# Kernel tuning notes

Hardware: AMD Instinct MI355X
Metric: run time of the kernel (lower is better)

Reference implementation:

```python
import jax, jax.numpy as jnp
import numpy as np

B, S, NC, ND, V = 16, 512, 10000, 10000, 128


def _rn(k, shape, scale=0.05):
    return jax.random.normal(k, shape, dtype=jnp.float32) * scale


def setup_inputs() -> dict:
    key = jax.random.key(0)
    ks = jax.random.split(key, 24)
    inp = {
        'c_seq': jax.random.randint(ks[0], (B, S), 0, NC),
        'd_seq': jax.random.randint(ks[1], (B, S), 0, ND),
        'r_seq': jax.random.uniform(ks[2], (B, S), dtype=jnp.float32),
        # embeddings / vectors
        'D1_w': _rn(ks[3], (ND, 1)),
        'D2_w': _rn(ks[4], (ND, V)),
        'v_r': _rn(ks[5], (V,)),
        'v_beta': _rn(ks[6], (V,)),
        # GRU (torch layout: gates ordered r,z,n; W_ih [3V,2V], W_hh [3V,V])
        'W_ih': _rn(ks[7], (3 * V, 2 * V)),
        'W_hh': _rn(ks[8], (3 * V, V)),
        'b_ih': jnp.zeros((3 * V,), jnp.float32),
        'b_hh': jnp.zeros((3 * V,), jnp.float32),
        # linear_1: V -> V -> V -> 1 (weights stored [in, out])
        'm1_W1': _rn(ks[9], (V, V)), 'm1_b1': jnp.zeros((V,), jnp.float32),
        'm1_W2': _rn(ks[10], (V, V)), 'm1_b2': jnp.zeros((V,), jnp.float32),
        'm1_W3': _rn(ks[11], (V, 1)), 'm1_b3': jnp.zeros((1,), jnp.float32),
        # linear_2: 3V -> V -> V -> 1
        'm2_W1': _rn(ks[12], (3 * V, V)), 'm2_b1': jnp.zeros((V,), jnp.float32),
        'm2_W2': _rn(ks[13], (V, V)), 'm2_b2': jnp.zeros((V,), jnp.float32),
        'm2_W3': _rn(ks[14], (V, 1)), 'm2_b3': jnp.zeros((1,), jnp.float32),
    }
    return inp


def _mlp(x, W1, b1, W2, b2, W3, b3):
    h = jax.nn.relu(x @ W1 + b1)
    h = jax.nn.relu(h @ W2 + b2)
    return h @ W3 + b3


def _gru_seq(x, W_ih, W_hh, b_ih, b_hh):
    # x: [B,S,2V] -> h_seq [B,S,V]; torch GRU gate order r,z,n
    xp = x @ W_ih.T + b_ih  # [B,S,3V]

    def step(h, xt):
        hp = h @ W_hh.T + b_hh
        xr, xz, xn = jnp.split(xt, 3, axis=-1)
        hr, hz, hn = jnp.split(hp, 3, axis=-1)
        r = jax.nn.sigmoid(xr + hr)
        z = jax.nn.sigmoid(xz + hz)
        n = jnp.tanh(xn + r * hn)
        h_new = (1.0 - z) * n + z * h
        return h_new, h_new

    h0 = jnp.zeros((x.shape[0], W_hh.shape[1]), x.dtype)
    _, hs = jax.lax.scan(step, h0, jnp.swapaxes(xp, 0, 1))  # [S,B,V]
    return jnp.swapaxes(hs, 0, 1)


def reference(c_seq, d_seq, r_seq, D1_w, D2_w, v_r, v_beta,
              W_ih, W_hh, b_ih, b_hh,
              m1_W1, m1_b1, m1_W2, m1_b2, m1_W3, m1_b3,
              m2_W1, m2_b1, m2_W2, m2_b2, m2_W3, m2_b3):
    v_d_seq = D2_w[d_seq]                     # [B,S,V]
    v_r_seq = r_seq[..., None] * v_r          # [B,S,V]

    h_seq = _gru_seq(jnp.concatenate([v_d_seq, v_r_seq], axis=-1),
                     W_ih, W_hh, b_ih, b_hh)  # [B,S,V]
    alpha_seq = _mlp(h_seq, m1_W1, m1_b1, m1_W2, m1_b2, m1_W3, m1_b3)[..., 0]  # [B,S]

    bidx = jnp.arange(c_seq.shape[0])

    def step(C, ins):
        c_t, vd_t, vr_t = ins                 # [B], [B,V], [B,V]
        beta_prev = C[bidx, c_t]              # gather: [B]
        v_beta_prev = beta_prev[:, None] * v_beta  # [B,V]
        new_c = _mlp(jnp.concatenate([v_beta_prev, vd_t, vr_t], axis=-1),
                     m2_W1, m2_b1, m2_W2, m2_b2, m2_W3, m2_b3)[:, 0]  # [B]
        C = C.at[bidx, c_t].set(new_c)        # scatter
        return C, (C, new_c)

    C0 = jnp.zeros((c_seq.shape[0], NC), jnp.float32)
    _, (C_seq, beta_seq) = jax.lax.scan(
        step, C0,
        (jnp.swapaxes(c_seq, 0, 1), jnp.swapaxes(v_d_seq, 0, 1), jnp.swapaxes(v_r_seq, 0, 1)))
    C_seq = jnp.swapaxes(C_seq, 0, 1)[..., None]   # [B,S,NC,1]
    beta_seq = jnp.swapaxes(beta_seq, 0, 1)        # [B,S]

    gamma_seq = D1_w[d_seq][..., 0]                # [B,S]
    return (alpha_seq, beta_seq, gamma_seq, h_seq, C_seq)
```

## Files before the change

kernel.cpp:

```cpp
#include <hip/hip_runtime.h>

#define Bq   16
#define Sq   512
#define Vq   128
#define NCq  10000

typedef __attribute__((ext_vector_type(8))) short short8v;
typedef __attribute__((ext_vector_type(4))) float f32x4;

#define OFF_XPF    0u
#define OFF_P1F    3145728u
#define OFF_WTIH   4194304u
#define OFF_WVRIH  4243456u
#define OFF_WVR1   4243840u
#define OFF_WVB    4243968u
#define OFF_W2T    4244096u
#define OFF_LIST   4260480u
#define OFF_CNT    4276864u

#define PLN 136
#define PLSZ (16*PLN+8)
#define SLOTB 6144
#define LSLOT 8192

__device__ __forceinline__ unsigned cvt_pk_bf16(float a, float b) {
    unsigned r;
    asm("v_cvt_pk_bf16_f32 %0, %1, %2" : "=v"(r) : "v"(a), "v"(b));
    return r;
}
__device__ __forceinline__ void barrier_lgkm() {
    asm volatile("s_waitcnt lgkmcnt(0)" ::: "memory");
    __builtin_amdgcn_sched_barrier(0);
    __builtin_amdgcn_s_barrier();
    __builtin_amdgcn_sched_barrier(0);
}
__device__ __forceinline__ void wait_vm8() {
    asm volatile("s_waitcnt vmcnt(8)" ::: "memory");
    __builtin_amdgcn_sched_barrier(0);
}
__device__ __forceinline__ void gload_lds16(const void* g, void* l) {
    __builtin_amdgcn_global_load_lds(
        (const __attribute__((address_space(1))) unsigned int*)g,
        (__attribute__((address_space(3))) unsigned int*)l, 16, 0, 0);
}

__global__ __launch_bounds__(256) void k0_prep(
    const int* __restrict__ c_seq, const int* __restrict__ d_seq,
    const float* __restrict__ D1_w,
    const float* __restrict__ W_ih,
    const float* __restrict__ v_r, const float* __restrict__ v_beta,
    const float* __restrict__ m2W1, const float* __restrict__ m2W2,
    float* __restrict__ ws, float* __restrict__ gamma_out)
{
    const int blk = blockIdx.x, tid = threadIdx.x;

    if (blk < 128) {
        float* WTIH = ws + OFF_WTIH;
        int base = blk * 384;
        for (int i = tid; i < 384; i += 256) {
            int e = base + i;
            int k = e / 384, g = e % 384;
            WTIH[e] = W_ih[g * 256 + k];
        }
    } else if (blk == 128) {
        float* WVRIH = ws + OFF_WVRIH;
        float* WVR1  = ws + OFF_WVR1;
        float* WVB   = ws + OFF_WVB;
        for (int g = tid; g < 384; g += 256) {
            float a = 0.f;
            for (int k = 0; k < 128; ++k) a = fmaf(v_r[k], W_ih[g * 256 + 128 + k], a);
            WVRIH[g] = a;
        }
        if (tid < 128) {
            float a = 0.f, b = 0.f;
            for (int k = 0; k < 128; ++k) {
                a = fmaf(v_r[k],    m2W1[(256 + k) * 128 + tid], a);
                b = fmaf(v_beta[k], m2W1[k * 128 + tid],         b);
            }
            WVR1[tid] = a; WVB[tid] = b;
        }
    } else if (blk < 145) {
        const int b = blk - 129;
        __shared__ int cs[Sq];
        __shared__ int po[Sq];
        for (int i = tid; i < Sq; i += 256) cs[i] = c_seq[b * Sq + i];
        __syncthreads();
        for (int t = tid; t < Sq; t += 256) {
            int c = cs[t];
            int p = -1;
            for (int u = t - 1; u >= 0; --u) if (cs[u] == c) { p = u; break; }
            po[t] = p;
        }
        __syncthreads();
        if (tid == 0) {
            int2* L = (int2*)(ws + OFF_LIST) + b * 512;
            int n = 0;
            for (int t = 0; t < Sq; ++t)
                if (po[t] >= 0) { L[n] = make_int2(t, po[t]); ++n; }
            ((int*)(ws + OFF_CNT))[b] = n;
        }
    } else if (blk < 161) {
        const int b = blk - 145;
        for (int s = tid; s < Sq; s += 256)
            gamma_out[b * Sq + s] = D1_w[d_seq[b * Sq + s]];
    } else {
        float* W2T = ws + OFF_W2T;
        for (int i = tid; i < 16384; i += 256) {
            int j = i >> 7, k = i & 127;
            W2T[i] = m2W2[k * 128 + j];
        }
    }
}

__global__ __launch_bounds__(256) void k1_gemm(
    const int* __restrict__ d_seq, const float* __restrict__ D2_w,
    const float* __restrict__ m2W1,
    const float* __restrict__ b_ih, const float* __restrict__ b_hh,
    const float* __restrict__ r_seq, const float* __restrict__ m2b1,
    float* __restrict__ ws)
{
    __shared__ float As[64 * 128];
    __shared__ float Bs[128 * 64];
    const int blk = blockIdx.x, tid = threadIdx.x;
    const int nc = blk & 7;
    const int m0 = (blk >> 3) * 64;
    const float* WTIH = ws + OFF_WTIH;

    const float4* D2v = (const float4*)D2_w;
    for (int e = tid; e < 2048; e += 256) {
        int r = e >> 5, q = e & 31;
        int d = d_seq[m0 + r];
        *(float4*)&As[r * 128 + 4 * q] = D2v[d * 32 + q];
    }
    for (int e = tid; e < 2048; e += 256) {
        int k = e >> 4, q = e & 15;
        float4 v;
        if (nc < 6) v = *(const float4*)&WTIH[k * 384 + nc * 64 + 4 * q];
        else        v = *(const float4*)&m2W1[(128 + k) * 128 + (nc - 6) * 64 + 4 * q];
        *(float4*)&Bs[k * 64 + 4 * q] = v;
    }
    __syncthreads();

    const int tx = tid & 15, ty = tid >> 4;
    const int c0 = 4 * tx, r0 = 4 * ty;
    float acc[4][4];
#pragma unroll
    for (int i = 0; i < 4; ++i)
#pragma unroll
        for (int j = 0; j < 4; ++j) acc[i][j] = 0.f;

    for (int k = 0; k < 128; ++k) {
        float4 bv = *(const float4*)&Bs[k * 64 + c0];
#pragma unroll
        for (int i = 0; i < 4; ++i) {
            float a = As[(r0 + i) * 128 + k];
            acc[i][0] = fmaf(a, bv.x, acc[i][0]);
            acc[i][1] = fmaf(a, bv.y, acc[i][1]);
            acc[i][2] = fmaf(a, bv.z, acc[i][2]);
            acc[i][3] = fmaf(a, bv.w, acc[i][3]);
        }
    }

    float rsv[4];
#pragma unroll
    for (int i = 0; i < 4; ++i) rsv[i] = r_seq[m0 + r0 + i];

    if (nc < 6) {
        const int grow0 = nc * 64 + c0;
        float4 bi  = *(const float4*)&b_ih[grow0];
        float4 wv4 = *(const float4*)&(ws + OFF_WVRIH)[grow0];
        float4 bh4 = make_float4(0.f, 0.f, 0.f, 0.f);
        if (nc < 4) bh4 = *(const float4*)&b_hh[grow0];
        float* XPF = ws + OFF_XPF;
        const int r4 = grow0 >> 2;
#pragma unroll
        for (int i = 0; i < 4; ++i) {
            int row = m0 + r0 + i;
            int t = row & 511, bb = row >> 9;
            float4 v;
            v.x = acc[i][0] + bi.x + bh4.x + rsv[i] * wv4.x;
            v.y = acc[i][1] + bi.y + bh4.y + rsv[i] * wv4.y;
            v.z = acc[i][2] + bi.z + bh4.z + rsv[i] * wv4.z;
            v.w = acc[i][3] + bi.w + bh4.w + rsv[i] * wv4.w;
            *(float4*)&XPF[((size_t)((bb >> 2) * 512 + t)) * 1536 + r4 * 16 + (bb & 3) * 4] = v;
        }
    } else {
        const int j0 = (nc - 6) * 64 + c0;
        float4 b1v = *(const float4*)&m2b1[j0];
        float4 wr1 = *(const float4*)&(ws + OFF_WVR1)[j0];
        float* P1F = ws + OFF_P1F;
#pragma unroll
        for (int i = 0; i < 4; ++i) {
            int row = m0 + r0 + i;
            int t = row & 511, bb = row >> 9;
            float4 v;
            v.x = acc[i][0] + b1v.x + rsv[i] * wr1.x;
            v.y = acc[i][1] + b1v.y + rsv[i] * wr1.y;
            v.z = acc[i][2] + b1v.z + rsv[i] * wr1.z;
            v.w = acc[i][3] + b1v.w + rsv[i] * wr1.w;
            *(float4*)&P1F[((size_t)(t * 16 + bb)) * 128 + j0] = v;
        }
    }
}

__global__ __launch_bounds__(256, 1) void k2_scan(
    const float* __restrict__ W_hh, const float* __restrict__ b_hh,
    const float* __restrict__ m2b2, const float* __restrict__ m2W3,
    const float* __restrict__ m2b3,
    float* __restrict__ ws,
    float* __restrict__ hseq_out, float* __restrict__ beta_out)
{
    __shared__ __align__(16) unsigned char smem[107040];
    const int tid = threadIdx.x;
    const int l = tid & 63, wv = tid >> 6;
    const int qq = l >> 4, cb = l & 15;
    const int bgid = blockIdx.x;

    if (bgid < 4) {
        unsigned short* hP  = (unsigned short*)smem;
        unsigned char*  xsl = smem + 8736;
        float* hstage = (float*)(smem + 8736 + 65536);
        const float* XPF = ws + OFF_XPF;
        const unsigned char* XPB = (const unsigned char*)XPF;

        short8v aH[2][3][4];
#pragma unroll
        for (int sub = 0; sub < 2; ++sub) {
            const int rg = 2 * wv + sub;
#pragma unroll
            for (int g = 0; g < 3; ++g) {
                const float* wrow = W_hh + (g * 128 + 16 * rg + cb) * 128;
#pragma unroll
                for (int kf = 0; kf < 4; ++kf) {
                    short8v h;
#pragma unroll
                    for (int e = 0; e < 8; ++e) {
                        unsigned u = __builtin_bit_cast(unsigned, wrow[kf * 32 + qq * 8 + e]);
                        h[e] = (short)((u + 0x7fffu + ((u >> 16) & 1u)) >> 16);
                    }
                    aH[sub][g][kf] = h;
                }
            }
        }
        f32x4 bhn4[2];
#pragma unroll
        for (int sub = 0; sub < 2; ++sub) {
            float4 t4 = *(const float4*)&b_hh[256 + 16 * (2 * wv + sub) + 4 * qq];
            bhn4[sub][0] = t4.x; bhn4[sub][1] = t4.y; bhn4[sub][2] = t4.z; bhn4[sub][3] = t4.w;
        }

        float hold[2][4];
#pragma unroll
        for (int sub = 0; sub < 2; ++sub)
#pragma unroll
            for (int i = 0; i < 4; ++i) hold[sub][i] = 0.f;

        for (int i = tid; i < 2 * PLSZ; i += 256) hP[i] = 0;
#pragma unroll
        for (int s = 0; s < 5; ++s) {
            const unsigned char* gsrc = XPB + ((size_t)(bgid * 512 + s)) * SLOTB;
            gload_lds16(gsrc + tid * 16, xsl + s * LSLOT + tid * 16);
            gload_lds16(gsrc + 4096 + tid * 16, xsl + s * LSLOT + 4096 + tid * 16);
        }
        __syncthreads();

        const float NL2E = -1.44269504f, L2E2 = 2.88539008f;
        for (int t = 0; t < 512; ++t) {
            if (t < 507) {
                const unsigned char* gsrc = XPB + ((size_t)(bgid * 512 + t + 5)) * SLOTB;
                unsigned char* dst = xsl + ((t + 5) & 7) * LSLOT;
                gload_lds16(gsrc + tid * 16, dst + tid * 16);
                gload_lds16(gsrc + 4096 + tid * 16, dst + 4096 + tid * 16);
            }
            if ((t & 7) == 0 && t > 0) {
                const float* hb = hstage + (((t >> 3) + 1) & 1) * 4096;
#pragma unroll
                for (int r2 = 0; r2 < 4; ++r2) {
                    int e2 = tid * 4 + r2;
                    int ss = e2 >> 7, rem = e2 & 127;
                    int bq2 = rem >> 5, q = rem & 31;
                    float4 v = *(const float4*)&hb[(ss * 4 + bq2) * 128 + q * 4];
                    *(float4*)&hseq_out[((size_t)((bgid * 4 + bq2) * 512 + (t - 8 + ss))) * 128 + q * 4] = v;
                }
            }

            const float* xc = (const float*)(xsl + (t & 7) * LSLOT) + (cb & 3) * 4;
            const unsigned short* HI = hP + (t & 1) * PLSZ;
            unsigned short* HIn = hP + ((t + 1) & 1) * PLSZ;

            f32x4 px2s[2];
            f32x4 C[2][3];
#pragma unroll
            for (int sub = 0; sub < 2; ++sub) {
                const int rg = 2 * wv + sub;
                C[sub][0] = *(const f32x4*)(xc + (0 * 32 + rg * 4 + qq) * 16);
                C[sub][1] = *(const f32x4*)(xc + (1 * 32 + rg * 4 + qq) * 16);
                px2s[sub] = *(const f32x4*)(xc + (2 * 32 + rg * 4 + qq) * 16);
                C[sub][2] = bhn4[sub];
            }
#pragma unroll
            for (int kf = 0; kf < 4; ++kf) {
                short8v B = *(const short8v*)(HI + cb * PLN + kf * 32 + qq * 8);
#pragma unroll
                for (int sub = 0; sub < 2; ++sub) {
                    C[sub][0] = __builtin_amdgcn_mfma_f32_16x16x32_bf16(aH[sub][0][kf], B, C[sub][0], 0, 0, 0);
                    C[sub][1] = __builtin_amdgcn_mfma_f32_16x16x32_bf16(aH[sub][1][kf], B, C[sub][1], 0, 0, 0);
                    C[sub][2] = __builtin_amdgcn_mfma_f32_16x16x32_bf16(aH[sub][2][kf], B, C[sub][2], 0, 0, 0);
                }
            }
            float hnew[2][4];
#pragma unroll
            for (int sub = 0; sub < 2; ++sub) {
#pragma unroll
                for (int i = 0; i < 4; ++i) {
                    float pr = C[sub][0][i];
                    float pz = C[sub][1][i];
                    float hn = C[sub][2][i];
                    float r = __builtin_amdgcn_rcpf(1.f + __builtin_amdgcn_exp2f(pr * NL2E));
                    float z = __builtin_amdgcn_rcpf(1.f + __builtin_amdgcn_exp2f(pz * NL2E));
                    float npre = fmaf(r, hn, px2s[sub][i]);
                    float n = fmaf(-2.f, __builtin_amdgcn_rcpf(1.f + __builtin_amdgcn_exp2f(npre * L2E2)), 1.f);
                    float hv = fmaf(z, hold[sub][i] - n, n);
                    hold[sub][i] = hv;
                    hnew[sub][i] = hv;
                }
            }
            if (cb < 4) {
                float* hst = hstage + ((t >> 3) & 1) * 4096;
#pragma unroll
                for (int sub = 0; sub < 2; ++sub) {
                    const int rg = 2 * wv + sub;
                    *(float4*)&hst[((t & 7) * 4 + cb) * 128 + 16 * rg + 4 * qq] =
                        make_float4(hnew[sub][0], hnew[sub][1], hnew[sub][2], hnew[sub][3]);
                    uint2 hw;
                    hw.x = cvt_pk_bf16(hnew[sub][0], hnew[sub][1]);
                    hw.y = cvt_pk_bf16(hnew[sub][2], hnew[sub][3]);
                    *(uint2*)(HIn + cb * PLN + 16 * rg + 4 * qq) = hw;
                }
            }
            wait_vm8();
            barrier_lgkm();
        }
#pragma unroll
        for (int r2 = 0; r2 < 4; ++r2) {
            int e2 = tid * 4 + r2;
            int ss = e2 >> 7, rem = e2 & 127;
            int bq2 = rem >> 5, q = rem & 31;
            float4 v = *(const float4*)&hstage[4096 + (ss * 4 + bq2) * 128 + q * 4];
            *(float4*)&hseq_out[((size_t)((bgid * 4 + bq2) * 512 + (504 + ss))) * 128 + q * 4] = v;
        }
    } else {
        const int d = bgid - 4;
        float* h1L = (float*)smem;
        const float* P1F = ws + OFF_P1F;
        const float* W2T = ws + OFF_W2T;

        const float* src = P1F + (size_t)d * 2048;
        for (int i = tid; i < 512; i += 256) {
            float4 v = *(const float4*)&src[i * 4];
            v.x = fmaxf(v.x, 0.f); v.y = fmaxf(v.y, 0.f);
            v.z = fmaxf(v.z, 0.f); v.w = fmaxf(v.w, 0.f);
            *(float4*)&h1L[i * 4] = v;
        }
        __syncthreads();

        const int r = tid >> 4, jg = tid & 15;
        float acc[8];
#pragma unroll
        for (int jj = 0; jj < 8; ++jj) acc[jj] = m2b2[jg * 8 + jj];
        for (int k4 = 0; k4 < 32; ++k4) {
            float4 h4 = *(const float4*)&h1L[r * 128 + k4 * 4];
#pragma unroll
            for (int jj = 0; jj < 8; ++jj) {
                float4 w4 = *(const float4*)&W2T[(jg * 8 + jj) * 128 + k4 * 4];
                acc[jj] = fmaf(h4.x, w4.x, acc[jj]);
                acc[jj] = fmaf(h4.y, w4.y, acc[jj]);
                acc[jj] = fmaf(h4.z, w4.z, acc[jj]);
                acc[jj] = fmaf(h4.w, w4.w, acc[jj]);
            }
        }
        float part = 0.f;
#pragma unroll
        for (int jj = 0; jj < 8; ++jj)
            part = fmaf(fmaxf(acc[jj], 0.f), m2W3[jg * 8 + jj], part);
        part += __shfl_xor(part, 1);
        part += __shfl_xor(part, 2);
        part += __shfl_xor(part, 4);
        part += __shfl_xor(part, 8);
        if (jg == 0) {
            int R = d * 16 + r;
            beta_out[(R & 15) * 512 + (R >> 4)] = part + m2b3[0];
        }
    }
}

__global__ __launch_bounds__(256, 1) void k2c_fix(
    const float* __restrict__ m2b2, const float* __restrict__ m2W3,
    const float* __restrict__ m2b3,
    float* __restrict__ ws, float* __restrict__ beta_out)
{
    __shared__ float W2L[128 * 129];
    __shared__ float betaF[512];
    __shared__ float h1L[128];
    __shared__ float red2[2];
    const int b = blockIdx.x, tid = threadIdx.x;
    const float* W2T = ws + OFF_W2T;
    const float* P1F = ws + OFF_P1F;

    for (int i = tid; i < 16384; i += 256) {
        int j = i >> 7, k = i & 127;
        W2L[j * 129 + k] = W2T[i];
    }
    for (int i = tid; i < 512; i += 256) betaF[i] = beta_out[b * 512 + i];

    const bool pa = tid < 128;
    float wvbj = 0.f, b2j = 0.f, w3j = 0.f;
    if (pa) {
        wvbj = (ws + OFF_WVB)[tid];
        b2j  = m2b2[tid];
        w3j  = m2W3[tid];
    }
    const float b3v = m2b3[0];
    const int n = ((const int*)(ws + OFF_CNT))[b];
    const int2* L = (const int2*)(ws + OFF_LIST) + b * 512;
    __syncthreads();

    for (int i = 0; i < n; ++i) {
        int2 tp = L[i];
        if (pa) {
            float bp = betaF[tp.y];
            float p1 = P1F[((size_t)(tp.x * 16 + b)) * 128 + tid];
            h1L[tid] = fmaxf(0.f, fmaf(bp, wvbj, p1));
        }
        barrier_lgkm();
        if (pa) {
            float a = b2j;
            const float* wr = &W2L[tid * 129];
            for (int k = 0; k < 128; ++k) a = fmaf(wr[k], h1L[k], a);
            float part = fmaxf(a, 0.f) * w3j;
#pragma unroll
            for (int off = 1; off < 64; off <<= 1) part += __shfl_xor(part, off);
            if ((tid & 63) == 0) red2[tid >> 6] = part;
        }
        barrier_lgkm();
        if (tid == 0) {
            float bta = red2[0] + red2[1] + b3v;
            betaF[tp.x] = bta;
            beta_out[b * 512 + tp.x] = bta;
        }
        barrier_lgkm();
    }
}

__global__ __launch_bounds__(256) void k2b_fill(
    const int* __restrict__ c_seq, const float* __restrict__ beta_in,
    float* __restrict__ C_out)
{
    __shared__ int   scs[Sq];
    __shared__ float sbt[Sq];
    const int bid = blockIdx.x, tid = threadIdx.x;
    const int b = bid / 40, rem = bid % 40;
    const int chunk = rem >> 2, q = rem & 3;

    for (int i = tid; i < Sq; i += 256) {
        scs[i] = c_seq[b * Sq + i];
        sbt[i] = beta_in[b * Sq + i];
    }
    __syncthreads();

    const int c0 = chunk * 1024 + tid * 4;
    if (c0 >= NCq) return;

    float cur0 = 0.f, cur1 = 0.f, cur2 = 0.f, cur3 = 0.f;
    const int tlo = q * 128, thi = tlo + 128;
    float* base = C_out + (size_t)b * Sq * NCq + c0;

    for (int t = 0; t < tlo; ++t) {
        int ct = scs[t] - c0; float bv = sbt[t];
        cur0 = (ct == 0) ? bv : cur0;
        cur1 = (ct == 1) ? bv : cur1;
        cur2 = (ct == 2) ? bv : cur2;
        cur3 = (ct == 3) ? bv : cur3;
    }
    for (int t = tlo; t < thi; ++t) {
        int ct = scs[t] - c0; float bv = sbt[t];
        cur0 = (ct == 0) ? bv : cur0;
        cur1 = (ct == 1) ? bv : cur1;
        cur2 = (ct == 2) ? bv : cur2;
        cur3 = (ct == 3) ? bv : cur3;
        *(float4*)(base + (size_t)t * NCq) = make_float4(cur0, cur1, cur2, cur3);
    }
}

__global__ __launch_bounds__(256) void k3_alpha(
    const float* __restrict__ hseq,
    const float* __restrict__ W1, const float* __restrict__ b1,
    const float* __restrict__ W2, const float* __restrict__ b2,
    const float* __restrict__ W3, const float* __restrict__ b3,
    float* __restrict__ alpha_out)
{
    __shared__ float Hs[32 * 128];
    __shared__ float T1[32 * 128];
    __shared__ float red[4][16];
    const int blk = blockIdx.x, tid = threadIdx.x;
    const int row0 = blk * 32;

    for (int e = tid; e < 1024; e += 256) {
        int r = e >> 5, q = e & 31;
        *(float4*)&Hs[r * 128 + 4 * q] =
            *(const float4*)&hseq[(size_t)(row0 + r) * 128 + 4 * q];
    }
    __syncthreads();

    const int j = tid & 127, rh = tid >> 7;
    const float b1j = b1[j], b2j = b2[j], w3j = W3[j];
    float acc[16];
#pragma unroll
    for (int r = 0; r < 16; ++r) acc[r] = b1j;
    for (int k = 0; k < 128; ++k) {
        float w = W1[k * 128 + j];
#pragma unroll
        for (int r = 0; r < 16; ++r)
            acc[r] = fmaf(Hs[(rh * 16 + r) * 128 + k], w, acc[r]);
    }
#pragma unroll
    for (int r = 0; r < 16; ++r) {
        acc[r] = fmaxf(acc[r], 0.f);
        T1[(rh * 16 + r) * 128 + j] = acc[r];
    }
    __syncthreads();
    float acc2[16];
#pragma unroll
    for (int r = 0; r < 16; ++r) acc2[r] = b2j;
    for (int k = 0; k < 128; ++k) {
        float w = W2[k * 128 + j];
#pragma unroll
        for (int r = 0; r < 16; ++r)
            acc2[r] = fmaf(T1[(rh * 16 + r) * 128 + k], w, acc2[r]);
    }
#pragma unroll
    for (int r = 0; r < 16; ++r) {
        float p = fmaxf(acc2[r], 0.f) * w3j;
#pragma unroll
        for (int off = 1; off < 64; off <<= 1) p += __shfl_xor(p, off);
        if ((tid & 63) == 0) red[tid >> 6][r] = p;
    }
    __syncthreads();
    if (tid < 32) {
        int rr = tid & 15, g = tid >> 4;
        alpha_out[row0 + g * 16 + rr] = red[2 * g][rr] + red[2 * g + 1][rr] + b3[0];
    }
}

extern "C" void kernel_launch(void* const* d_in, const int* in_sizes, int n_in,
                              void* d_out, int out_size, void* d_ws, size_t ws_size,
                              hipStream_t stream) {
    const int*   c_seq = (const int*)d_in[0];
    const int*   d_seq = (const int*)d_in[1];
    const float* r_seq = (const float*)d_in[2];
    const float* D1_w  = (const float*)d_in[3];
    const float* D2_w  = (const float*)d_in[4];
    const float* v_r   = (const float*)d_in[5];
    const float* v_b   = (const float*)d_in[6];
    const float* W_ih  = (const float*)d_in[7];
    const float* W_hh  = (const float*)d_in[8];
    const float* b_ih  = (const float*)d_in[9];
    const float* b_hh  = (const float*)d_in[10];
    const float* m1W1  = (const float*)d_in[11];
    const float* m1b1  = (const float*)d_in[12];
    const float* m1W2  = (const float*)d_in[13];
    const float* m1b2  = (const float*)d_in[14];
    const float* m1W3  = (const float*)d_in[15];
    const float* m1b3  = (const float*)d_in[16];
    const float* m2W1  = (const float*)d_in[17];
    const float* m2b1  = (const float*)d_in[18];
    const float* m2W2  = (const float*)d_in[19];
    const float* m2b2  = (const float*)d_in[20];
    const float* m2W3  = (const float*)d_in[21];
    const float* m2b3  = (const float*)d_in[22];

    float* out   = (float*)d_out;
    float* alpha = out;
    float* beta  = out + 8192;
    float* gamma = out + 16384;
    float* hseq  = out + 24576;
    float* Cseq  = out + 1073152;
    float* ws    = (float*)d_ws;

    hipLaunchKernelGGL(k0_prep, dim3(162), dim3(256), 0, stream,
                       c_seq, d_seq, D1_w, W_ih, v_r, v_b, m2W1, m2W2, ws, gamma);
    hipLaunchKernelGGL(k1_gemm, dim3(1024), dim3(256), 0, stream,
                       d_seq, D2_w, m2W1, b_ih, b_hh, r_seq, m2b1, ws);
    hipLaunchKernelGGL(k2_scan, dim3(516), dim3(256), 0, stream,
                       W_hh, b_hh, m2b2, m2W3, m2b3, ws, hseq, beta);
    hipLaunchKernelGGL(k2c_fix, dim3(16), dim3(256), 0, stream,
                       m2b2, m2W3, m2b3, ws, beta);
    hipLaunchKernelGGL(k2b_fill, dim3(640), dim3(256), 0, stream,
                       c_seq, beta, Cseq);
    hipLaunchKernelGGL(k3_alpha, dim3(256), dim3(256), 0, stream,
                       hseq, m1W1, m1b1, m1W2, m1b2, m1W3, m1b3, alpha);
}
```

Baseline: 699.4 us.

## Overlap GRU scan with C fill by reorganizing beta compute and fix kernels

Splits the old scan kernel: the independent beta MLP blocks and the sequential beta fix-up now run in one kernel, with fix-up blocks spin-waiting on a global atomic counter until all beta blocks finish. The GRU scan blocks are then co-scheduled with the C_seq fill blocks in a single kernel, so the large C_seq write overlaps the latency-bound recurrence. This removes kernel launches and the serial gap between the scan and the fill. The spin-wait assumes every producer block gets scheduled, and a sync counter written in k0_prep is incremented but never read for the second slot.

```diff
diff --git a/kernel.cpp b/kernel.cpp
--- a/kernel.cpp
+++ b/kernel.cpp
@@ -17,6 +17,7 @@
 #define OFF_W2T    4244096u
 #define OFF_LIST   4260480u
 #define OFF_CNT    4276864u
+#define OFF_SYNC   4276880u
 
 #define PLN 136
 #define PLSZ (16*PLN+8)
@@ -79,6 +80,8 @@
             }
             WVR1[tid] = a; WVB[tid] = b;
         }
+        if (tid == 200) ((int*)(ws + OFF_SYNC))[0] = 0;
+        if (tid == 201) ((int*)(ws + OFF_SYNC))[1] = 0;
     } else if (blk < 145) {
         const int b = blk - 129;
         __shared__ int cs[Sq];
@@ -203,12 +206,128 @@
     }
 }
 
-__global__ __launch_bounds__(256, 1) void k2_scan(
-    const float* __restrict__ W_hh, const float* __restrict__ b_hh,
+__global__ __launch_bounds__(256, 1) void ka_beta(
     const float* __restrict__ m2b2, const float* __restrict__ m2W3,
     const float* __restrict__ m2b3,
+    float* __restrict__ ws, float* __restrict__ beta_out)
+{
+    __shared__ __align__(16) unsigned char smem[68664];
+    const int bid = blockIdx.x, tid = threadIdx.x;
+    int* cnt0 = (int*)(ws + OFF_SYNC);
+
+    if (bid < 512) {
+        float* h1L = (float*)smem;
+        const float* P1F = ws + OFF_P1F;
+        const float* W2T = ws + OFF_W2T;
+
+        const float* src = P1F + (size_t)bid * 2048;
+        for (int i = tid; i < 512; i += 256) {
+            float4 v = *(const float4*)&src[i * 4];
+            v.x = fmaxf(v.x, 0.f); v.y = fmaxf(v.y, 0.f);
+            v.z = fmaxf(v.z, 0.f); v.w = fmaxf(v.w, 0.f);
+            *(float4*)&h1L[i * 4] = v;
+        }
+        __syncthreads();
+
+        const int r = tid >> 4, jg = tid & 15;
+        float acc[8];
+#pragma unroll
+        for (int jj = 0; jj < 8; ++jj) acc[jj] = m2b2[jg * 8 + jj];
+        for (int k4 = 0; k4 < 32; ++k4) {
+            float4 h4 = *(const float4*)&h1L[r * 128 + k4 * 4];
+#pragma unroll
+            for (int jj = 0; jj < 8; ++jj) {
+                float4 w4 = *(const float4*)&W2T[(jg * 8 + jj) * 128 + k4 * 4];
+                acc[jj] = fmaf(h4.x, w4.x, acc[jj]);
+                acc[jj] = fmaf(h4.y, w4.y, acc[jj]);
+                acc[jj] = fmaf(h4.z, w4.z, acc[jj]);
+                acc[jj] = fmaf(h4.w, w4.w, acc[jj]);
+            }
+        }
+        float part = 0.f;
+#pragma unroll
+        for (int jj = 0; jj < 8; ++jj)
+            part = fmaf(fmaxf(acc[jj], 0.f), m2W3[jg * 8 + jj], part);
+        part += __shfl_xor(part, 1);
+        part += __shfl_xor(part, 2);
+        part += __shfl_xor(part, 4);
+        part += __shfl_xor(part, 8);
+        if (jg == 0) {
+            int R = bid * 16 + r;
+            beta_out[(R & 15) * 512 + (R >> 4)] = part + m2b3[0];
+        }
+        __threadfence();
+        __syncthreads();
+        if (tid == 0)
+            __hip_atomic_fetch_add(cnt0, 1, __ATOMIC_RELEASE, __HIP_MEMORY_SCOPE_AGENT);
+    } else {
+        const int b = bid - 512;
+        while (__hip_atomic_load(cnt0, __ATOMIC_ACQUIRE, __HIP_MEMORY_SCOPE_AGENT) < 512)
+            __builtin_amdgcn_s_sleep(2);
+        __syncthreads();
+
+        float* W2L = (float*)smem;
+        float* betaF = (float*)(smem + 66048);
+        float* h1L = (float*)(smem + 66048 + 2048);
+        float* red2 = (float*)(smem + 66048 + 2048 + 512);
+        const float* W2T = ws + OFF_W2T;
+        const float* P1F = ws + OFF_P1F;
+
+        for (int i = tid; i < 16384; i += 256) {
+            int j = i >> 7, k = i & 127;
+            W2L[j * 129 + k] = W2T[i];
+        }
+        for (int i = tid; i < 512; i += 256) betaF[i] = beta_out[b * 512 + i];
+
+        const bool pa = tid < 128;
+        float wvbj = 0.f, b2j = 0.f, w3j = 0.f;
+        if (pa) {
+            wvbj = (ws + OFF_WVB)[tid];
+            b2j  = m2b2[tid];
+            w3j  = m2W3[tid];
+        }
+        const float b3v = m2b3[0];
+        const int n = ((const int*)(ws + OFF_CNT))[b];
+        const int2* L = (const int2*)(ws + OFF_LIST) + b * 512;
+        __syncthreads();
+
+        for (int i = 0; i < n; ++i) {
+            int2 tp = L[i];
+            if (pa) {
+                float bp = betaF[tp.y];
+                float p1 = P1F[((size_t)(tp.x * 16 + b)) * 128 + tid];
+                h1L[tid] = fmaxf(0.f, fmaf(bp, wvbj, p1));
+            }
+            barrier_lgkm();
+            if (pa) {
+                float a = b2j;
+                const float* wr = &W2L[tid * 129];
+                for (int k = 0; k < 128; ++k) a = fmaf(wr[k], h1L[k], a);
+                float part = fmaxf(a, 0.f) * w3j;
+#pragma unroll
+                for (int off = 1; off < 64; off <<= 1) part += __shfl_xor(part, off);
+                if ((tid & 63) == 0) red2[tid >> 6] = part;
+            }
+            barrier_lgkm();
+            if (tid == 0) {
+                float bta = red2[0] + red2[1] + b3v;
+                betaF[tp.x] = bta;
+                beta_out[b * 512 + tp.x] = bta;
+            }
+            barrier_lgkm();
+        }
+        if (tid == 0) {
+            __threadfence();
+            __hip_atomic_fetch_add(cnt0 + 1, 1, __ATOMIC_RELEASE, __HIP_MEMORY_SCOPE_AGENT);
+        }
+    }
+}
+
+__global__ __launch_bounds__(256, 1) void kb_main(
+    const float* __restrict__ W_hh, const float* __restrict__ b_hh,
+    const int* __restrict__ c_seq, const float* __restrict__ beta_in,
     float* __restrict__ ws,
-    float* __restrict__ hseq_out, float* __restrict__ beta_out)
+    float* __restrict__ hseq_out, float* __restrict__ C_out)
 {
     __shared__ __align__(16) unsigned char smem[107040];
     const int tid = threadIdx.x;
@@ -350,145 +469,40 @@
             *(float4*)&hseq_out[((size_t)((bgid * 4 + bq2) * 512 + (504 + ss))) * 128 + q * 4] = v;
         }
     } else {
-        const int d = bgid - 4;
-        float* h1L = (float*)smem;
-        const float* P1F = ws + OFF_P1F;
-        const float* W2T = ws + OFF_W2T;
-
-        const float* src = P1F + (size_t)d * 2048;
-        for (int i = tid; i < 512; i += 256) {
-            float4 v = *(const float4*)&src[i * 4];
-            v.x = fmaxf(v.x, 0.f); v.y = fmaxf(v.y, 0.f);
-            v.z = fmaxf(v.z, 0.f); v.w = fmaxf(v.w, 0.f);
-            *(float4*)&h1L[i * 4] = v;
-        }
-        __syncthreads();
-
-        const int r = tid >> 4, jg = tid & 15;
-        float acc[8];
-#pragma unroll
-        for (int jj = 0; jj < 8; ++jj) acc[jj] = m2b2[jg * 8 + jj];
-        for (int k4 = 0; k4 < 32; ++k4) {
-            float4 h4 = *(const float4*)&h1L[r * 128 + k4 * 4];
-#pragma unroll
-            for (int jj = 0; jj < 8; ++jj) {
-                float4 w4 = *(const float4*)&W2T[(jg * 8 + jj) * 128 + k4 * 4];
-                acc[jj] = fmaf(h4.x, w4.x, acc[jj]);
-                acc[jj] = fmaf(h4.y, w4.y, acc[jj]);
-                acc[jj] = fmaf(h4.z, w4.z, acc[jj]);
-                acc[jj] = fmaf(h4.w, w4.w, acc[jj]);
-            }
-        }
-        float part = 0.f;
-#pragma unroll
-        for (int jj = 0; jj < 8; ++jj)
-            part = fmaf(fmaxf(acc[jj], 0.f), m2W3[jg * 8 + jj], part);
-        part += __shfl_xor(part, 1);
-        part += __shfl_xor(part, 2);
-        part += __shfl_xor(part, 4);
-        part += __shfl_xor(part, 8);
-        if (jg == 0) {
-            int R = d * 16 + r;
-            beta_out[(R & 15) * 512 + (R >> 4)] = part + m2b3[0];
-        }
-    }
-}
-
-__global__ __launch_bounds__(256, 1) void k2c_fix(
-    const float* __restrict__ m2b2, const float* __restrict__ m2W3,
-    const float* __restrict__ m2b3,
-    float* __restrict__ ws, float* __restrict__ beta_out)
-{
-    __shared__ float W2L[128 * 129];
-    __shared__ float betaF[512];
-    __shared__ float h1L[128];
-    __shared__ float red2[2];
-    const int b = blockIdx.x, tid = threadIdx.x;
-    const float* W2T = ws + OFF_W2T;
-    const float* P1F = ws + OFF_P1F;
-
-    for (int i = tid; i < 16384; i += 256) {
-        int j = i >> 7, k = i & 127;
-        W2L[j * 129 + k] = W2T[i];
-    }
-    for (int i = tid; i < 512; i += 256) betaF[i] = beta_out[b * 512 + i];
-
-    const bool pa = tid < 128;
-    float wvbj = 0.f, b2j = 0.f, w3j = 0.f;
-    if (pa) {
-        wvbj = (ws + OFF_WVB)[tid];
-        b2j  = m2b2[tid];
-        w3j  = m2W3[tid];
-    }
-    const float b3v = m2b3[0];
-    const int n = ((const int*)(ws + OFF_CNT))[b];
-    const int2* L = (const int2*)(ws + OFF_LIST) + b * 512;
-    __syncthreads();
-
-    for (int i = 0; i < n; ++i) {
-        int2 tp = L[i];
-        if (pa) {
-            float bp = betaF[tp.y];
-            float p1 = P1F[((size_t)(tp.x * 16 + b)) * 128 + tid];
-            h1L[tid] = fmaxf(0.f, fmaf(bp, wvbj, p1));
-        }
-        barrier_lgkm();
-        if (pa) {
-            float a = b2j;
-            const float* wr = &W2L[tid * 129];
-            for (int k = 0; k < 128; ++k) a = fmaf(wr[k], h1L[k], a);
-            float part = fmaxf(a, 0.f) * w3j;
-#pragma unroll
-            for (int off = 1; off < 64; off <<= 1) part += __shfl_xor(part, off);
-            if ((tid & 63) == 0) red2[tid >> 6] = part;
-        }
-        barrier_lgkm();
-        if (tid == 0) {
-            float bta = red2[0] + red2[1] + b3v;
-            betaF[tp.x] = bta;
-            beta_out[b * 512 + tp.x] = bta;
-        }
-        barrier_lgkm();
-    }
-}
-
-__global__ __launch_bounds__(256) void k2b_fill(
-    const int* __restrict__ c_seq, const float* __restrict__ beta_in,
-    float* __restrict__ C_out)
-{
-    __shared__ int   scs[Sq];
-    __shared__ float sbt[Sq];
-    const int bid = blockIdx.x, tid = threadIdx.x;
-    const int b = bid / 40, rem = bid % 40;
-    const int chunk = rem >> 2, q = rem & 3;
-
-    for (int i = tid; i < Sq; i += 256) {
-        scs[i] = c_seq[b * Sq + i];
-        sbt[i] = beta_in[b * Sq + i];
-    }
-    __syncthreads();
-
-    const int c0 = chunk * 1024 + tid * 4;
-    if (c0 >= NCq) return;
-
-    float cur0 = 0.f, cur1 = 0.f, cur2 = 0.f, cur3 = 0.f;
-    const int tlo = q * 128, thi = tlo + 128;
-    float* base = C_out + (size_t)b * Sq * NCq + c0;
-
-    for (int t = 0; t < tlo; ++t) {
-        int ct = scs[t] - c0; float bv = sbt[t];
-        cur0 = (ct == 0) ? bv : cur0;
-        cur1 = (ct == 1) ? bv : cur1;
-        cur2 = (ct == 2) ? bv : cur2;
-        cur3 = (ct == 3) ? bv : cur3;
-    }
-    for (int t = tlo; t < thi; ++t) {
-        int ct = scs[t] - c0; float bv = sbt[t];
-        cur0 = (ct == 0) ? bv : cur0;
-        cur1 = (ct == 1) ? bv : cur1;
-        cur2 = (ct == 2) ? bv : cur2;
-        cur3 = (ct == 3) ? bv : cur3;
-        *(float4*)(base + (size_t)t * NCq) = make_float4(cur0, cur1, cur2, cur3);
+        int* scs = (int*)smem;
+        float* sbt = (float*)(smem + 2048);
+        const int z = bgid - 4;
+        const int b = z / 40, rem = z % 40;
+        const int chunk = rem >> 2, q = rem & 3;
+
+        for (int i = tid; i < Sq; i += 256) {
+            scs[i] = c_seq[b * Sq + i];
+            sbt[i] = beta_in[b * Sq + i];
+        }
+        __syncthreads();
+
+        const int c0 = chunk * 1024 + tid * 4;
+        if (c0 >= NCq) return;
+
+        float cur0 = 0.f, cur1 = 0.f, cur2 = 0.f, cur3 = 0.f;
+        const int tlo = q * 128, thi = tlo + 128;
+        float* base = C_out + (size_t)b * Sq * NCq + c0;
+
+        for (int t = 0; t < tlo; ++t) {
+            int ct = scs[t] - c0; float bv = sbt[t];
+            cur0 = (ct == 0) ? bv : cur0;
+            cur1 = (ct == 1) ? bv : cur1;
+            cur2 = (ct == 2) ? bv : cur2;
+            cur3 = (ct == 3) ? bv : cur3;
+        }
+        for (int t = tlo; t < thi; ++t) {
+            int ct = scs[t] - c0; float bv = sbt[t];
+            cur0 = (ct == 0) ? bv : cur0;
+            cur1 = (ct == 1) ? bv : cur1;
+            cur2 = (ct == 2) ? bv : cur2;
+            cur3 = (ct == 3) ? bv : cur3;
+            *(float4*)(base + (size_t)t * NCq) = make_float4(cur0, cur1, cur2, cur3);
+        }
     }
 }
 
@@ -591,12 +605,10 @@
                        c_seq, d_seq, D1_w, W_ih, v_r, v_b, m2W1, m2W2, ws, gamma);
     hipLaunchKernelGGL(k1_gemm, dim3(1024), dim3(256), 0, stream,
                        d_seq, D2_w, m2W1, b_ih, b_hh, r_seq, m2b1, ws);
-    hipLaunchKernelGGL(k2_scan, dim3(516), dim3(256), 0, stream,
-                       W_hh, b_hh, m2b2, m2W3, m2b3, ws, hseq, beta);
-    hipLaunchKernelGGL(k2c_fix, dim3(16), dim3(256), 0, stream,
+    hipLaunchKernelGGL(ka_beta, dim3(528), dim3(256), 0, stream,
                        m2b2, m2W3, m2b3, ws, beta);
-    hipLaunchKernelGGL(k2b_fill, dim3(640), dim3(256), 0, stream,
-                       c_seq, beta, Cseq);
+    hipLaunchKernelGGL(kb_main, dim3(644), dim3(256), 0, stream,
+                       W_hh, b_hh, c_seq, beta, ws, hseq, Cseq);
     hipLaunchKernelGGL(k3_alpha, dim3(256), dim3(256), 0, stream,
                        hseq, m1W1, m1b1, m1W2, m1b2, m1W3, m1b3, alpha);
 }
```

Result: slower. 759.3 us (+8.6%).
